# Kernel tuning notes

Hardware: AMD Instinct MI355X
Metric: run time of the kernel (lower is better)

The kernel has to match this reference:

```python
import jax, jax.numpy as jnp
import numpy as np

B, H, L = 256, 1024, 4
HQ, HKV, D = 16, 8, 64
I, V, C = 4096, 1027, 16
EPS = 1e-6
TEMP, TOP_P, TOP_K = 0.8, 0.6, 30
REP_PEN, REP_WIN = 1.1, 50


def _rms(x, w):
    return x * jax.lax.rsqrt(jnp.mean(x * x, axis=-1, keepdims=True) + EPS) * w


def _layer(h, wi, wq, wk, wv, qn, kn, wo, wp, wg, wu, wd):
    # h: [B,1,H]. seq_len == 1; RoPE at position 0 is identity (cos=1, sin=0).
    r = h
    x = _rms(h, wi)
    q = _rms((x @ wq).reshape(B, 1, HQ, D), qn)   # Qwen3 per-head q_norm
    k = _rms((x @ wk).reshape(B, 1, HKV, D), kn)  # Qwen3 per-head k_norm
    v = (x @ wv).reshape(B, 1, HKV, D)
    g = HQ // HKV
    kr = jnp.repeat(k, g, axis=2)
    vr = jnp.repeat(v, g, axis=2)
    s = jnp.einsum('bqhd,bkhd->bhqk', q, kr) / float(np.sqrt(D))
    a = jax.nn.softmax(s, axis=-1)
    o = jnp.einsum('bhqk,bkhd->bqhd', a, vr).reshape(B, 1, HQ * D) @ wo
    h = r + o
    r = h
    x = _rms(h, wp)
    m = (jax.nn.silu(x @ wg) * (x @ wu)) @ wd  # SwiGLU MLP
    return r + m


def _rep_penalty(scores, hist):
    # scores: [B,V], hist: [B,W] int token ids
    cur = jnp.take_along_axis(scores, hist, axis=1)
    new = jnp.where(cur < 0, cur * REP_PEN, cur / REP_PEN)
    return scores.at[jnp.arange(B)[:, None], hist].set(new)


def _sample(logits, key):
    l = logits / TEMP
    # top-k mask
    thr = jax.lax.top_k(l, TOP_K)[0][:, -1:]
    l = jnp.where(l < thr, -jnp.inf, l)
    # top-p: sort ascending, drop lowest-cumulative-prob <= 1 - top_p
    order = jnp.argsort(l, axis=-1)
    sl = jnp.take_along_axis(l, order, axis=1)
    cp = jnp.cumsum(jax.nn.softmax(sl, axis=-1), axis=-1)
    smask = cp <= 1.0 - TOP_P
    mask = jnp.zeros_like(l, dtype=bool).at[jnp.arange(B)[:, None], order].set(smask)
    l = jnp.where(mask, -jnp.inf, l)
    return jax.random.categorical(key, l, axis=-1)


def setup_inputs() -> dict:
    key = jax.random.key(0)
    ks = jax.random.split(key, 12)
    s = 0.02
    return {
        'backbone_hidden': jax.random.normal(ks[0], (B, 1, H), jnp.float32),
        'generated_history': jax.random.randint(ks[1], (B, 200, C), 0, V),
        'gen_step': 100,
        'embed_tables': jax.random.normal(ks[2], (C, V, H), jnp.float32) * s,
        'lm_heads': jax.random.normal(ks[3], (C, V, H), jnp.float32) * s,
        'w_in_norm': jnp.ones((L, H), jnp.float32),
        'w_q': jax.random.normal(ks[4], (L, H, HQ * D), jnp.float32) * s,
        'w_k': jax.random.normal(ks[5], (L, H, HKV * D), jnp.float32) * s,
        'w_v': jax.random.normal(ks[6], (L, H, HKV * D), jnp.float32) * s,
        'q_norm': jnp.ones((L, D), jnp.float32),
        'k_norm': jnp.ones((L, D), jnp.float32),
        'w_o': jax.random.normal(ks[7], (L, HQ * D, H), jnp.float32) * s,
        'w_post_norm': jnp.ones((L, H), jnp.float32),
        'w_gate': jax.random.normal(ks[8], (L, H, I), jnp.float32) * s,
        'w_up': jax.random.normal(ks[9], (L, H, I), jnp.float32) * s,
        'w_down': jax.random.normal(ks[10], (L, I, H), jnp.float32) * s,
        'final_norm': jnp.ones((H,), jnp.float32),
    }


def reference(backbone_hidden, generated_history, gen_step, embed_tables, lm_heads,
              w_in_norm, w_q, w_k, w_v, q_norm, k_norm, w_o, w_post_norm,
              w_gate, w_up, w_down, final_norm):
    keys = jax.random.split(jax.random.key(1234), C)
    hidden = backbone_hidden  # [B,1,H]
    toks = []
    for i in range(C):  # 16 sequential codebook steps
        h = hidden
        for l in range(L):  # 4 decoder layers
            h = _layer(h, w_in_norm[l], w_q[l], w_k[l], w_v[l], q_norm[l],
                       k_norm[l], w_o[l], w_post_norm[l], w_gate[l],
                       w_up[l], w_down[l])
        h = _rms(h, final_norm)
        logits = h[:, -1, :] @ lm_heads[i].T  # [B,V]
        hist = generated_history[:, :gen_step, i][:, -REP_WIN:]
        logits = _rep_penalty(logits, hist)
        tok = _sample(logits, keys[i])  # [B]
        toks.append(tok)
        if i < C - 1:
            hidden = embed_tables[i + 1][tok][:, None, :]  # [B,1,H]
    return jnp.stack(toks, axis=1)  # [B,C] int tokens
```

## Files before the change

kernel.cpp:

```cpp
#include <hip/hip_runtime.h>
#include <cstdint>
#include <cfloat>
#include <cmath>


#define PARTITIONABLE 1

namespace {
constexpr int B = 256, H = 1024, L = 4;
constexpr int I = 4096, V = 1027, C = 16;
constexpr int KV = 512;
}

__device__ __forceinline__ void tf2x32(uint32_t k0, uint32_t k1,
                                       uint32_t x0, uint32_t x1,
                                       uint32_t& o0, uint32_t& o1) {
  uint32_t k2 = k0 ^ k1 ^ 0x1BD11BDAu;
  x0 += k0; x1 += k1;
#define TFR(r) { x0 += x1; x1 = (x1 << r) | (x1 >> (32 - r)); x1 ^= x0; }
  TFR(13) TFR(15) TFR(26) TFR(6)
  x0 += k1; x1 += k2 + 1u;
  TFR(17) TFR(29) TFR(16) TFR(24)
  x0 += k2; x1 += k0 + 2u;
  TFR(13) TFR(15) TFR(26) TFR(6)
  x0 += k0; x1 += k1 + 3u;
  TFR(17) TFR(29) TFR(16) TFR(24)
  x0 += k1; x1 += k2 + 4u;
  TFR(13) TFR(15) TFR(26) TFR(6)
  x0 += k2; x1 += k0 + 5u;
#undef TFR
  o0 = x0; o1 = x1;
}

__device__ __forceinline__ float gumbel_for(uint32_t k0, uint32_t k1,
                                            uint32_t idx) {
  uint32_t o0, o1, bits;
  tf2x32(k0, k1, 0u, idx, o0, o1);
  bits = o0 ^ o1;
  float f = __uint_as_float((bits >> 9) | 0x3f800000u) - 1.0f;
  float u = fmaxf(FLT_MIN, f + FLT_MIN);
  return -logf(-logf(u));
}

__global__ __launch_bounds__(256) void copy_rms_k(const float* __restrict__ src,
                                                  float* __restrict__ h,
                                                  float* __restrict__ r) {
  int b = blockIdx.x, tid = threadIdx.x;
  float4 v = *(const float4*)&src[(size_t)b * H + tid * 4];
  *(float4*)&h[(size_t)b * H + tid * 4] = v;
  float s = v.x * v.x + v.y * v.y + v.z * v.z + v.w * v.w;
  for (int off = 32; off > 0; off >>= 1) s += __shfl_down(s, off, 64);
  __shared__ float red[4];
  if ((tid & 63) == 0) red[tid >> 6] = s;
  __syncthreads();
  if (tid == 0) {
    float t = red[0] + red[1] + red[2] + red[3];
    r[b] = 1.0f / sqrtf(t * (1.0f / 1024.0f) + 1e-6f);
  }
}

__global__ __launch_bounds__(256) void fold_k(const float* __restrict__ wo,
                                              float* __restrict__ wof) {
  int blk = blockIdx.x;
  int l = blk >> 9, c = blk & 511;
  int kb = c >> 6, jl = c & 63;
  const float* w = wo + (size_t)l * H * H;
  int k1 = kb * 128 + jl, k2 = k1 + 64;
  int j = threadIdx.x * 4;
  float4 a = *(const float4*)&w[(size_t)k1 * H + j];
  float4 bq = *(const float4*)&w[(size_t)k2 * H + j];
  float4 o = {a.x + bq.x, a.y + bq.y, a.z + bq.z, a.w + bq.w};
  *(float4*)&wof[((size_t)l * KV + c) * H + j] = o;
}

template <bool NORM, bool GATHER, bool BT, bool BOUND>
__global__ __launch_bounds__(256) void gemm64_k(
    const float* __restrict__ A, int lda,
    const float* __restrict__ rv, const float* __restrict__ wn,
    const float* __restrict__ Bm, int ldb,
    float* __restrict__ Cp, int N, int Kslice) {
  __shared__ __align__(16) float As[32][68];
  __shared__ __align__(16) float Bs[32][68];
  const int tid = threadIdx.x;
  const int tx = tid & 15, ty = tid >> 4;
  const int bm = blockIdx.y * 64;
  const int bn = blockIdx.x * 64;
  const int ks0 = blockIdx.z * Kslice;
  float4 acc[4];
#pragma unroll
  for (int i = 0; i < 4; ++i) acc[i] = float4{0.f, 0.f, 0.f, 0.f};

  for (int k0 = 0; k0 < Kslice; k0 += 32) {
    const int kbase = ks0 + k0;
#pragma unroll
    for (int s = 0; s < 2; ++s) {
      int slot = tid + s * 256;
      int rI = slot >> 3, c = slot & 7;
      int k = kbase + c * 4;
      int col = GATHER ? (((k >> 7) << 6) | (k & 63)) : k;
      float4 av = *(const float4*)&A[(size_t)(bm + rI) * lda + col];
      if (NORM) {
        float sc = rv[bm + rI];
        float4 wv = *(const float4*)&wn[k];
        av.x *= sc * wv.x; av.y *= sc * wv.y;
        av.z *= sc * wv.z; av.w *= sc * wv.w;
      }
      As[c * 4 + 0][rI] = av.x; As[c * 4 + 1][rI] = av.y;
      As[c * 4 + 2][rI] = av.z; As[c * 4 + 3][rI] = av.w;
    }
#pragma unroll
    for (int s = 0; s < 2; ++s) {
      int slot = tid + s * 256;
      if (!BT) {
        int kI = slot >> 4, c4 = slot & 15;
        float4 bv = *(const float4*)&Bm[(size_t)(kbase + kI) * ldb + bn + c4 * 4];
        *(float4*)&Bs[kI][c4 * 4] = bv;
      } else {
        int nI = slot >> 3, c = slot & 7;
        int n = bn + nI;
        float4 bv = {0.f, 0.f, 0.f, 0.f};
        if (!BOUND || n < N)
          bv = *(const float4*)&Bm[(size_t)n * ldb + kbase + c * 4];
        Bs[c * 4 + 0][nI] = bv.x; Bs[c * 4 + 1][nI] = bv.y;
        Bs[c * 4 + 2][nI] = bv.z; Bs[c * 4 + 3][nI] = bv.w;
      }
    }
    __syncthreads();
#pragma unroll
    for (int kk = 0; kk < 32; ++kk) {
      float4 a = *(const float4*)&As[kk][ty * 4];
      float4 b = *(const float4*)&Bs[kk][tx * 4];
      float ar[4] = {a.x, a.y, a.z, a.w};
#pragma unroll
      for (int i = 0; i < 4; ++i) {
        acc[i].x = fmaf(ar[i], b.x, acc[i].x);
        acc[i].y = fmaf(ar[i], b.y, acc[i].y);
        acc[i].z = fmaf(ar[i], b.z, acc[i].z);
        acc[i].w = fmaf(ar[i], b.w, acc[i].w);
      }
    }
    __syncthreads();
  }
  float* base = Cp + (size_t)blockIdx.z * 256 * N;
#pragma unroll
  for (int i = 0; i < 4; ++i) {
    int row = bm + ty * 4 + i;
    int colb = bn + tx * 4;
    if (!BOUND) {
      *(float4*)&base[(size_t)row * N + colb] = acc[i];
    } else {
      float vals[4] = {acc[i].x, acc[i].y, acc[i].z, acc[i].w};
      for (int j = 0; j < 4; ++j)
        if (colb + j < N) base[(size_t)row * N + colb + j] = vals[j];
    }
  }
}

__global__ __launch_bounds__(256) void gemm_gu_k(
    const float* __restrict__ hm, const float* __restrict__ rv,
    const float* __restrict__ wn,
    const float* __restrict__ Bg, const float* __restrict__ Bu,
    float* __restrict__ Mo) {
  __shared__ __align__(16) float As[32][68];
  __shared__ __align__(16) float Gs[32][36];
  __shared__ __align__(16) float Us[32][36];
  const int tid = threadIdx.x;
  const int tx = tid & 15, ty = tid >> 4;
  const int bm = blockIdx.y * 64;
  const int bn = blockIdx.x * 32;
  float2 ag[4], au[4];
#pragma unroll
  for (int i = 0; i < 4; ++i) { ag[i] = float2{0.f, 0.f}; au[i] = float2{0.f, 0.f}; }

  for (int k0 = 0; k0 < H; k0 += 32) {
#pragma unroll
    for (int s = 0; s < 2; ++s) {
      int slot = tid + s * 256;
      int rI = slot >> 3, c = slot & 7;
      int k = k0 + c * 4;
      float4 av = *(const float4*)&hm[(size_t)(bm + rI) * H + k];
      float sc = rv[bm + rI];
      float4 wv = *(const float4*)&wn[k];
      av.x *= sc * wv.x; av.y *= sc * wv.y;
      av.z *= sc * wv.z; av.w *= sc * wv.w;
      As[c * 4 + 0][rI] = av.x; As[c * 4 + 1][rI] = av.y;
      As[c * 4 + 2][rI] = av.z; As[c * 4 + 3][rI] = av.w;
    }
    {
      int kI = tid >> 3, c4 = tid & 7;
      float4 gv = *(const float4*)&Bg[(size_t)(k0 + kI) * I + bn + c4 * 4];
      float4 uv = *(const float4*)&Bu[(size_t)(k0 + kI) * I + bn + c4 * 4];
      *(float4*)&Gs[kI][c4 * 4] = gv;
      *(float4*)&Us[kI][c4 * 4] = uv;
    }
    __syncthreads();
#pragma unroll
    for (int kk = 0; kk < 32; ++kk) {
      float4 a = *(const float4*)&As[kk][ty * 4];
      float2 g = *(const float2*)&Gs[kk][tx * 2];
      float2 u = *(const float2*)&Us[kk][tx * 2];
      float ar[4] = {a.x, a.y, a.z, a.w};
#pragma unroll
      for (int i = 0; i < 4; ++i) {
        ag[i].x = fmaf(ar[i], g.x, ag[i].x);
        ag[i].y = fmaf(ar[i], g.y, ag[i].y);
        au[i].x = fmaf(ar[i], u.x, au[i].x);
        au[i].y = fmaf(ar[i], u.y, au[i].y);
      }
    }
    __syncthreads();
  }
#pragma unroll
  for (int i = 0; i < 4; ++i) {
    int row = bm + ty * 4 + i;
    int col = bn + tx * 2;
    float g0 = ag[i].x, g1 = ag[i].y;
    float s0 = 1.0f / (1.0f + expf(-g0));
    float s1 = 1.0f / (1.0f + expf(-g1));
    float2 o = {g0 * s0 * au[i].x, g1 * s1 * au[i].y};
    *(float2*)&Mo[(size_t)row * I + col] = o;
  }
}

__global__ __launch_bounds__(256) void red_v_k(const float* __restrict__ part,
                                               float* __restrict__ v, int S) {
  int i4 = (blockIdx.x * 256 + threadIdx.x) * 4;
  float4 s = {0.f, 0.f, 0.f, 0.f};
  for (int ss = 0; ss < S; ++ss) {
    float4 p = *(const float4*)&part[(size_t)ss * (256 * KV) + i4];
    s.x += p.x; s.y += p.y; s.z += p.z; s.w += p.w;
  }
  *(float4*)&v[i4] = s;
}

__global__ __launch_bounds__(256) void red_add_rms_k(const float* __restrict__ part,
                                                     float* __restrict__ h,
                                                     float* __restrict__ r, int S) {
  int b = blockIdx.x, tid = threadIdx.x;
  size_t off = (size_t)b * H + tid * 4;
  float4 a = *(const float4*)&h[off];
  for (int ss = 0; ss < S; ++ss) {
    float4 p = *(const float4*)&part[(size_t)ss * (256 * H) + off];
    a.x += p.x; a.y += p.y; a.z += p.z; a.w += p.w;
  }
  *(float4*)&h[off] = a;
  float s = a.x * a.x + a.y * a.y + a.z * a.z + a.w * a.w;
  for (int o = 32; o > 0; o >>= 1) s += __shfl_down(s, o, 64);
  __shared__ float red[4];
  if ((tid & 63) == 0) red[tid >> 6] = s;
  __syncthreads();
  if (tid == 0) {
    float t = red[0] + red[1] + red[2] + red[3];
    r[b] = 1.0f / sqrtf(t * (1.0f / 1024.0f) + 1e-6f);
  }
}

__global__ __launch_bounds__(256) void head_k(
    const float* __restrict__ part, int S,
    const int* __restrict__ gh, const int* __restrict__ gen_step_p,
    int step, const float* __restrict__ embed_next,
    float* __restrict__ h, float* __restrict__ r,
    int* __restrict__ out) {
  constexpr int TOPK = 30;
  constexpr int KMAX = 64;
  const int b = blockIdx.x, tid = threadIdx.x;
  __shared__ float sl[V];
  __shared__ float rv_[256]; __shared__ int ri[256];
  __shared__ float topv[TOPK]; __shared__ int topi[TOPK];
  __shared__ float kv[KMAX]; __shared__ int ki[KMAX]; __shared__ int keepf[KMAX];
  __shared__ uint32_t skey[2];
  __shared__ int scnt, sn, stok;
  __shared__ float redf[4];

  if (tid == 0) {
    uint32_t o0, o1;
    tf2x32(0u, 1234u, 0u, (uint32_t)step, o0, o1);
    skey[0] = o0; skey[1] = o1;
    scnt = 0;
  }
  for (int v = tid; v < V; v += 256) {
    float s = 0.f;
    for (int ss = 0; ss < S; ++ss)
      s += part[(size_t)ss * (256 * V) + (size_t)b * V + v];
    sl[v] = s;
  }
  __syncthreads();
  int gs = *gen_step_p;
  int cnt = gs < 50 ? gs : 50;
  int start = gs - cnt;
  int tkn = -1; float val = 0.f;
  if (tid < cnt) {
    tkn = gh[(size_t)b * 200 * C + (size_t)(start + tid) * C + step];
    val = sl[tkn];
  }
  __syncthreads();
  if (tid < cnt) sl[tkn] = (val < 0.f) ? val * 1.1f : val / 1.1f;
  __syncthreads();
  for (int v = tid; v < V; v += 256) sl[v] = sl[v] / 0.8f;
  __syncthreads();

  for (int it = 0; it < TOPK; ++it) {
    float bv = -INFINITY; int bi = 0x7fffffff;
    for (int v = tid; v < V; v += 256) {
      float x = sl[v];
      if (x > bv) { bv = x; bi = v; }
    }
    rv_[tid] = bv; ri[tid] = bi;
    __syncthreads();
    for (int s = 128; s > 0; s >>= 1) {
      if (tid < s) {
        float ov = rv_[tid + s]; int oi = ri[tid + s];
        if (ov > rv_[tid] || (ov == rv_[tid] && oi < ri[tid])) { rv_[tid] = ov; ri[tid] = oi; }
      }
      __syncthreads();
    }
    if (tid == 0) { topv[it] = rv_[0]; topi[it] = ri[0]; sl[ri[0]] = -INFINITY; }
    __syncthreads();
  }
  if (tid < TOPK) sl[topi[tid]] = topv[tid];
  __syncthreads();
  const float thr = topv[TOPK - 1];
  for (int v = tid; v < V; v += 256) {
    if (sl[v] >= thr) {
      int p = atomicAdd(&scnt, 1);
      if (p < KMAX) { kv[p] = sl[v]; ki[p] = v; }
    }
  }
  __syncthreads();

  if (tid == 0) {
    int n = scnt < KMAX ? scnt : KMAX;
    for (int a = 1; a < n; ++a) {
      float cv = kv[a]; int ci = ki[a];
      int p = a - 1;
      while (p >= 0 && (kv[p] > cv || (kv[p] == cv && ki[p] > ci))) {
        kv[p + 1] = kv[p]; ki[p + 1] = ki[p]; --p;
      }
      kv[p + 1] = cv; ki[p + 1] = ci;
    }
    float mx = kv[n - 1];
    float denom = 0.f;
    for (int j = 0; j < n; ++j) denom += expf(kv[j] - mx);
    float c = 0.f;
    for (int j = 0; j < n; ++j) {
      float p = expf(kv[j] - mx) / denom;
      c += p;
      keepf[j] = ((double)c > 0.4) ? 1 : 0;
    }
    sn = n;
  }
  __syncthreads();

  int n = sn;
  rv_[tid] = -INFINITY; ri[tid] = 0x7fffffff;
  if (tid < n && keepf[tid]) {
    uint32_t idx = (uint32_t)b * (uint32_t)V + (uint32_t)ki[tid];
    float g = gumbel_for(skey[0], skey[1], idx);
    rv_[tid] = kv[tid] + g;
    ri[tid] = ki[tid];
  }
  __syncthreads();
  for (int s = 128; s > 0; s >>= 1) {
    if (tid < s) {
      float ov = rv_[tid + s]; int oi = ri[tid + s];
      if (ov > rv_[tid] || (ov == rv_[tid] && oi < ri[tid])) { rv_[tid] = ov; ri[tid] = oi; }
    }
    __syncthreads();
  }
  if (tid == 0) {
    stok = ri[0];
    out[(size_t)b * C + step] = ri[0];
  }
  __syncthreads();

  if (embed_next != nullptr) {
    int tok = stok;
    float4 e = *(const float4*)&embed_next[(size_t)tok * H + tid * 4];
    *(float4*)&h[(size_t)b * H + tid * 4] = e;
    float s = e.x * e.x + e.y * e.y + e.z * e.z + e.w * e.w;
    for (int o = 32; o > 0; o >>= 1) s += __shfl_down(s, o, 64);
    if ((tid & 63) == 0) redf[tid >> 6] = s;
    __syncthreads();
    if (tid == 0) {
      float t = redf[0] + redf[1] + redf[2] + redf[3];
      r[b] = 1.0f / sqrtf(t * (1.0f / 1024.0f) + 1e-6f);
    }
  }
}

extern "C" void kernel_launch(void* const* d_in, const int* in_sizes, int n_in,
                              void* d_out, int out_size, void* d_ws, size_t ws_size,
                              hipStream_t stream) {
  const float* backbone = (const float*)d_in[0];
  const int*   gh       = (const int*)d_in[1];
  const int*   gen_step = (const int*)d_in[2];
  const float* embed    = (const float*)d_in[3];
  const float* lm       = (const float*)d_in[4];
  const float* w_in     = (const float*)d_in[5];
  const float* w_v      = (const float*)d_in[8];
  const float* w_o      = (const float*)d_in[11];
  const float* w_post   = (const float*)d_in[12];
  const float* w_g      = (const float*)d_in[13];
  const float* w_u      = (const float*)d_in[14];
  const float* w_d      = (const float*)d_in[15];
  const float* fnorm    = (const float*)d_in[16];
  int* out = (int*)d_out;
  float* ws = (float*)d_ws;

  const bool big = ws_size >= (size_t)22600000;
  float* h    = ws;
  float* v    = ws + 262144;
  float* m    = ws + 393216;
  float* wof  = big ? ws + 1441792 : nullptr;
  float* part = big ? ws + 3538944 : ws + 1441792;
  float* r    = big ? ws + 5642240 : ws + 1966080;

  const int S1 = big ? 16 : 4;
  const int S2 = big ? 8 : 2;
  const int S4 = big ? 8 : 2;
  const int S5 = big ? 8 : 1;

  copy_rms_k<<<dim3(256), dim3(256), 0, stream>>>(backbone, h, r);
  if (big) fold_k<<<dim3(2048), dim3(256), 0, stream>>>(w_o, wof);

  for (int i = 0; i < C; ++i) {
    for (int l = 0; l < L; ++l) {
      gemm64_k<true, false, false, false><<<dim3(8, 4, S1), dim3(256), 0, stream>>>(
          h, H, r, w_in + (size_t)l * H, w_v + (size_t)l * H * KV, KV,
          part, KV, H / S1);
      red_v_k<<<dim3(128), dim3(256), 0, stream>>>(part, v, S1);
      if (big)
        gemm64_k<false, false, false, false><<<dim3(16, 4, S2), dim3(256), 0, stream>>>(
            v, KV, nullptr, nullptr, wof + (size_t)l * KV * H, H,
            part, H, KV / S2);
      else
        gemm64_k<false, true, false, false><<<dim3(16, 4, S2), dim3(256), 0, stream>>>(
            v, KV, nullptr, nullptr, w_o + (size_t)l * H * H, H,
            part, H, H / S2);
      red_add_rms_k<<<dim3(256), dim3(256), 0, stream>>>(part, h, r, S2);
      gemm_gu_k<<<dim3(128, 4), dim3(256), 0, stream>>>(
          h, r, w_post + (size_t)l * H,
          w_g + (size_t)l * H * I, w_u + (size_t)l * H * I, m);
      gemm64_k<false, false, false, false><<<dim3(16, 4, S4), dim3(256), 0, stream>>>(
          m, I, nullptr, nullptr, w_d + (size_t)l * I * H, H,
          part, H, I / S4);
      red_add_rms_k<<<dim3(256), dim3(256), 0, stream>>>(part, h, r, S4);
    }
    gemm64_k<true, false, true, true><<<dim3(17, 4, S5), dim3(256), 0, stream>>>(
        h, H, r, fnorm, lm + (size_t)i * V * H, H, part, V, H / S5);
    head_k<<<dim3(256), dim3(256), 0, stream>>>(
        part, S5, gh, gen_step, i,
        (i < C - 1) ? embed + (size_t)(i + 1) * V * H : nullptr,
        h, r, out);
  }
}
```

Before: 10.66 ms.

## Widen gate/up GEMM tile to 64 columns and double-buffer LDS with register prefetch

The fused gate/up SwiGLU GEMM now computes a 64x64 output tile per block instead of 64x32. Each thread accumulates 4x4 results for both gate and up, so A-tile reuse and arithmetic intensity go up, and the grid halves to 64x4 blocks. The k-loop is software-pipelined: the next tile is loaded into registers during compute and written into a second LDS buffer, which removes one barrier per iteration. In exchange it uses more registers and LDS, which may lower occupancy, and launches only 256 blocks on a GPU with many CUs.

```diff
diff --git a/kernel.cpp b/kernel.cpp
--- a/kernel.cpp
+++ b/kernel.cpp
@@ -161,64 +161,95 @@
     const float* __restrict__ wn,
     const float* __restrict__ Bg, const float* __restrict__ Bu,
     float* __restrict__ Mo) {
-  __shared__ __align__(16) float As[32][68];
-  __shared__ __align__(16) float Gs[32][36];
-  __shared__ __align__(16) float Us[32][36];
+  __shared__ __align__(16) float As[2][32][68];
+  __shared__ __align__(16) float Gs[2][32][68];
+  __shared__ __align__(16) float Us[2][32][68];
   const int tid = threadIdx.x;
   const int tx = tid & 15, ty = tid >> 4;
   const int bm = blockIdx.y * 64;
-  const int bn = blockIdx.x * 32;
-  float2 ag[4], au[4];
-#pragma unroll
-  for (int i = 0; i < 4; ++i) { ag[i] = float2{0.f, 0.f}; au[i] = float2{0.f, 0.f}; }
-
-  for (int k0 = 0; k0 < H; k0 += 32) {
+  const int bn = blockIdx.x * 64;
+  float4 ag[4], au[4];
+#pragma unroll
+  for (int i = 0; i < 4; ++i) {
+    ag[i] = float4{0.f, 0.f, 0.f, 0.f};
+    au[i] = float4{0.f, 0.f, 0.f, 0.f};
+  }
+
+  float4 a_pre[2], g_pre[2], u_pre[2];
+
+  auto load_regs = [&](int k0) {
 #pragma unroll
     for (int s = 0; s < 2; ++s) {
-      int slot = tid + s * 256;
-      int rI = slot >> 3, c = slot & 7;
-      int k = k0 + c * 4;
+      const int slot = tid + s * 256;
+      const int rI = slot >> 3, c = slot & 7;
+      const int k = k0 + c * 4;
       float4 av = *(const float4*)&hm[(size_t)(bm + rI) * H + k];
-      float sc = rv[bm + rI];
-      float4 wv = *(const float4*)&wn[k];
+      const float sc = rv[bm + rI];
+      const float4 wv = *(const float4*)&wn[k];
       av.x *= sc * wv.x; av.y *= sc * wv.y;
       av.z *= sc * wv.z; av.w *= sc * wv.w;
-      As[c * 4 + 0][rI] = av.x; As[c * 4 + 1][rI] = av.y;
-      As[c * 4 + 2][rI] = av.z; As[c * 4 + 3][rI] = av.w;
-    }
-    {
-      int kI = tid >> 3, c4 = tid & 7;
-      float4 gv = *(const float4*)&Bg[(size_t)(k0 + kI) * I + bn + c4 * 4];
-      float4 uv = *(const float4*)&Bu[(size_t)(k0 + kI) * I + bn + c4 * 4];
-      *(float4*)&Gs[kI][c4 * 4] = gv;
-      *(float4*)&Us[kI][c4 * 4] = uv;
-    }
-    __syncthreads();
+      a_pre[s] = av;
+      const int kI = slot >> 4, c4 = slot & 15;
+      g_pre[s] = *(const float4*)&Bg[(size_t)(k0 + kI) * I + bn + c4 * 4];
+      u_pre[s] = *(const float4*)&Bu[(size_t)(k0 + kI) * I + bn + c4 * 4];
+    }
+  };
+  auto store_lds = [&](int p) {
+#pragma unroll
+    for (int s = 0; s < 2; ++s) {
+      const int slot = tid + s * 256;
+      const int rI = slot >> 3, c = slot & 7;
+      As[p][c * 4 + 0][rI] = a_pre[s].x;
+      As[p][c * 4 + 1][rI] = a_pre[s].y;
+      As[p][c * 4 + 2][rI] = a_pre[s].z;
+      As[p][c * 4 + 3][rI] = a_pre[s].w;
+      const int kI = slot >> 4, c4 = slot & 15;
+      *(float4*)&Gs[p][kI][c4 * 4] = g_pre[s];
+      *(float4*)&Us[p][kI][c4 * 4] = u_pre[s];
+    }
+  };
+
+  load_regs(0);
+  store_lds(0);
+  __syncthreads();
+  int p = 0;
+  for (int k0 = 0; k0 < H; k0 += 32) {
+    if (k0 + 32 < H) load_regs(k0 + 32);
 #pragma unroll
     for (int kk = 0; kk < 32; ++kk) {
-      float4 a = *(const float4*)&As[kk][ty * 4];
-      float2 g = *(const float2*)&Gs[kk][tx * 2];
-      float2 u = *(const float2*)&Us[kk][tx * 2];
-      float ar[4] = {a.x, a.y, a.z, a.w};
+      const float4 a = *(const float4*)&As[p][kk][ty * 4];
+      const float4 g = *(const float4*)&Gs[p][kk][tx * 4];
+      const float4 u = *(const float4*)&Us[p][kk][tx * 4];
+      const float ar[4] = {a.x, a.y, a.z, a.w};
 #pragma unroll
       for (int i = 0; i < 4; ++i) {
         ag[i].x = fmaf(ar[i], g.x, ag[i].x);
         ag[i].y = fmaf(ar[i], g.y, ag[i].y);
+        ag[i].z = fmaf(ar[i], g.z, ag[i].z);
+        ag[i].w = fmaf(ar[i], g.w, ag[i].w);
         au[i].x = fmaf(ar[i], u.x, au[i].x);
         au[i].y = fmaf(ar[i], u.y, au[i].y);
-      }
-    }
-    __syncthreads();
+        au[i].z = fmaf(ar[i], u.z, au[i].z);
+        au[i].w = fmaf(ar[i], u.w, au[i].w);
+      }
+    }
+    if (k0 + 32 < H) store_lds(p ^ 1);
+    __syncthreads();
+    p ^= 1;
   }
 #pragma unroll
   for (int i = 0; i < 4; ++i) {
-    int row = bm + ty * 4 + i;
-    int col = bn + tx * 2;
-    float g0 = ag[i].x, g1 = ag[i].y;
-    float s0 = 1.0f / (1.0f + expf(-g0));
-    float s1 = 1.0f / (1.0f + expf(-g1));
-    float2 o = {g0 * s0 * au[i].x, g1 * s1 * au[i].y};
-    *(float2*)&Mo[(size_t)row * I + col] = o;
+    const int row = bm + ty * 4 + i;
+    const int col = bn + tx * 4;
+    const float gv[4] = {ag[i].x, ag[i].y, ag[i].z, ag[i].w};
+    const float uv[4] = {au[i].x, au[i].y, au[i].z, au[i].w};
+    float o[4];
+#pragma unroll
+    for (int j = 0; j < 4; ++j) {
+      const float s = 1.0f / (1.0f + expf(-gv[j]));
+      o[j] = gv[j] * s * uv[j];
+    }
+    *(float4*)&Mo[(size_t)row * I + col] = *(const float4*)&o[0];
   }
 }
 
@@ -438,7 +469,7 @@
             v, KV, nullptr, nullptr, w_o + (size_t)l * H * H, H,
             part, H, H / S2);
       red_add_rms_k<<<dim3(256), dim3(256), 0, stream>>>(part, h, r, S2);
-      gemm_gu_k<<<dim3(128, 4), dim3(256), 0, stream>>>(
+      gemm_gu_k<<<dim3(64, 4), dim3(256), 0, stream>>>(
           h, r, w_post + (size_t)l * H,
           w_g + (size_t)l * H * I, w_u + (size_t)l * H * I, m);
       gemm64_k<false, false, false, false><<<dim3(16, 4, S4), dim3(256), 0, stream>>>(
```

Result: slower. 13.43 ms (+26.0%).
